# Kernel optimization log

Measured on AMD Instinct MI355X. Metric: run time of the kernel, lower is better.

The kernel has to match this reference:

```python
import jax, jax.numpy as jnp
import numpy as np

K = 32            # spatial kernel: neighbors per anchor
STRIDE = 4        # spatial_stride -> S = N // 4 anchors
TK_HALF = 1       # temporal_kernel_size=3 -> window offsets -1,0,+1


def setup_inputs() -> dict:
    key = jax.random.key(0)
    k1, k2, k3 = jax.random.split(key, 3)
    points = jax.random.normal(k1, (2, 4, 8192, 6), dtype=jnp.float32)
    # conv_d: Conv2d(4 -> 64, 1x1, bias=False) as a dense matrix [out,in]
    Wd = jax.random.normal(k2, (64, 4), dtype=jnp.float32) * 0.1
    # mlp: Conv2d(64 -> 128, 1x1, bias=False)
    Wm = jax.random.normal(k3, (128, 64), dtype=jnp.float32) * 0.1
    return {"points": points, "Wd": Wd, "Wm": Wm}


def _fps(xyz, npoint):
    """Farthest point sampling on a single frame. xyz: [N,3] -> idx [npoint] int32.
    Deterministic start at index 0."""
    d0 = jnp.sum((xyz - xyz[0]) ** 2, axis=-1)  # [N]

    def body(dists, _):
        nxt = jnp.argmax(dists)
        d = jnp.sum((xyz - xyz[nxt]) ** 2, axis=-1)
        return jnp.minimum(dists, d), nxt.astype(jnp.int32)

    _, idxs = jax.lax.scan(body, d0, None, length=npoint - 1)
    return jnp.concatenate([jnp.zeros((1,), jnp.int32), idxs])


def _knn_idx(neighbor_xyz, anchor_xyz, k):
    """Adaptive ball query realized as k-nearest-neighbors.
    neighbor_xyz: [B,N,3], anchor_xyz: [B,S,3] -> idx [B,S,k]."""
    d2 = jnp.sum((anchor_xyz[:, :, None, :] - neighbor_xyz[:, None, :, :]) ** 2, axis=-1)  # [B,S,N]
    _, idx = jax.lax.top_k(-d2, k)
    return idx


def _group(pts, idx):
    """pts: [B,N,C], idx: [B,S,K] -> [B,S,K,C] gather per batch."""
    return jax.vmap(lambda p, i: p[i])(pts, idx)


def reference(points, Wd, Wm):
    xyzs = points[..., :3]                       # [B,L,N,3] (rgb unused when in_planes==0)
    B, L, N, _ = xyzs.shape
    S = N // STRIDE
    # replicate temporal padding [1,1]
    pad = jnp.concatenate([xyzs[:, :1], xyzs, xyzs[:, -1:]], axis=1)  # [B,L+2,N,3]

    new_xyzs, new_feats = [], []
    for t in range(TK_HALF, L + 2 - TK_HALF):    # anchor frames in padded indexing
        frame = pad[:, t]                        # [B,N,3]
        aidx = jax.vmap(lambda x: _fps(x, S))(frame)       # [B,S]
        anchor = _group(frame, aidx[:, :, None])[:, :, 0]  # [B,S,3]

        fsum = jnp.zeros((B, S, Wm.shape[0]), dtype=points.dtype)
        for di in range(-TK_HALF, TK_HALF + 1):
            nb = pad[:, t + di]                              # [B,N,3]
            idx = _knn_idx(nb, anchor, K)                    # [B,S,K]
            grouped = _group(nb, idx)                        # [B,S,K,3]
            disp = grouped - anchor[:, :, None, :]           # xyz displacement
            tdisp = jnp.full((B, S, K, 1), float(di), dtype=points.dtype)
            d4 = jnp.concatenate([disp, tdisp], axis=-1)     # [B,S,K,4]
            h = jax.nn.relu(jnp.einsum('bskc,oc->bsko', d4, Wd))   # conv_d + ReLU
            h = jax.nn.relu(jnp.einsum('bsko,po->bskp', h, Wm))    # mlp + ReLU
            fsum = fsum + jnp.max(h, axis=2)                 # spatial max-pool, temporal sum
        new_xyzs.append(anchor)
        new_feats.append(fsum)

    new_xyzs = jnp.stack(new_xyzs, axis=1)                   # [B,T,S,3]
    new_feats = jnp.stack(new_feats, axis=1).transpose(0, 1, 3, 2)  # [B,T,C,S]
    return new_xyzs, new_feats
```

## Files before the change

### kernel.cpp

```cpp
#include <hip/hip_runtime.h>
#include <stdint.h>

#define NPTS 8192
#define NS   2048
#define KNNK 32

typedef unsigned long long u64;
typedef float f32x2 __attribute__((ext_vector_type(2)));

__device__ __forceinline__ float wave_max_f32_dpp(float x) {
    int t;
    t = __builtin_amdgcn_update_dpp(0, __float_as_int(x), 0xB1, 0xF, 0xF, false);
    x = fmaxf(x, __int_as_float(t));
    t = __builtin_amdgcn_update_dpp(0, __float_as_int(x), 0x4E, 0xF, 0xF, false);
    x = fmaxf(x, __int_as_float(t));
    t = __builtin_amdgcn_update_dpp(0, __float_as_int(x), 0x141, 0xF, 0xF, false);
    x = fmaxf(x, __int_as_float(t));
    t = __builtin_amdgcn_update_dpp(0, __float_as_int(x), 0x140, 0xF, 0xF, false);
    x = fmaxf(x, __int_as_float(t));
    t = __builtin_amdgcn_update_dpp(0, __float_as_int(x), 0x142, 0xF, 0xF, false);
    x = fmaxf(x, __int_as_float(t));
    t = __builtin_amdgcn_update_dpp(0, __float_as_int(x), 0x143, 0xF, 0xF, false);
    x = fmaxf(x, __int_as_float(t));
    return x;
}

__device__ __forceinline__ int wave_min_i32_dpp(int x) {
    const int INF = 0x7FFFFFFF;
    int t;
    t = __builtin_amdgcn_update_dpp(INF, x, 0xB1, 0xF, 0xF, false);
    x = t < x ? t : x;
    t = __builtin_amdgcn_update_dpp(INF, x, 0x4E, 0xF, 0xF, false);
    x = t < x ? t : x;
    t = __builtin_amdgcn_update_dpp(INF, x, 0x141, 0xF, 0xF, false);
    x = t < x ? t : x;
    t = __builtin_amdgcn_update_dpp(INF, x, 0x140, 0xF, 0xF, false);
    x = t < x ? t : x;
    t = __builtin_amdgcn_update_dpp(INF, x, 0x142, 0xF, 0xF, false);
    x = t < x ? t : x;
    t = __builtin_amdgcn_update_dpp(INF, x, 0x143, 0xF, 0xF, false);
    x = t < x ? t : x;
    return x;
}

__global__ __launch_bounds__(512)
void fps_kernel(const float* __restrict__ pts,
                float* __restrict__ out_xyz)
{
#pragma clang fp contract(off)
    const int bt  = blockIdx.x;
    const int tid = threadIdx.x;
    const float* frame = pts + (size_t)bt * NPTS * 6;

    __shared__ float4 p4[NPTS];
    __shared__ u64 ring[3];

    f32x2 x2[8], y2[8], z2[8], dd2[8];
#pragma unroll
    for (int j = 0; j < 16; ++j) {
        int n = j * 512 + tid;
        float x = frame[n*6+0], y = frame[n*6+1], z = frame[n*6+2];
        x2[j >> 1][j & 1] = x;
        y2[j >> 1][j & 1] = y;
        z2[j >> 1][j & 1] = z;
        dd2[j >> 1][j & 1] = 3.4028234663852886e38f;
        p4[n] = make_float4(x, y, z, 0.0f);
    }
    if (tid < 3) ring[tid] = 0;
    if (tid == 0) {
        float* ow = out_xyz + (size_t)bt * NS * 3;
        ow[0] = x2[0][0]; ow[1] = y2[0][0]; ow[2] = z2[0][0];
    }
    __syncthreads();
    float sx = p4[0].x, sy = p4[0].y, sz = p4[0].z;

    int r = 1;
    for (int i = 1; i < NS; ++i) {
        f32x2 sxv = {sx, sx}, syv = {sy, sy}, szv = {sz, sz};
        f32x2 m2 = {0.0f, 0.0f};
#pragma unroll
        for (int q = 0; q < 8; ++q) {
            f32x2 dx = x2[q] - sxv;
            f32x2 dy = y2[q] - syv;
            f32x2 dz = z2[q] - szv;
            f32x2 dd = (dx*dx + dy*dy) + dz*dz;
            f32x2 nd;
            nd[0] = fminf(dd2[q][0], dd[0]);
            nd[1] = fminf(dd2[q][1], dd[1]);
            dd2[q] = nd;
            m2[0] = fmaxf(m2[0], nd[0]);
            m2[1] = fmaxf(m2[1], nd[1]);
        }
        float mloc = fmaxf(m2[0], m2[1]);
        int bestn = 0;
#pragma unroll
        for (int j = 15; j >= 0; --j)
            bestn = (dd2[j >> 1][j & 1] == mloc) ? (j * 512 + tid) : bestn;
        float wM = wave_max_f32_dpp(mloc);
        float M = __int_as_float(__builtin_amdgcn_readlane(__float_as_int(wM), 63));
        int cand = (mloc == M) ? bestn : 0x7FFFFFFF;
        int wI = wave_min_i32_dpp(cand);
        int idxm = __builtin_amdgcn_readlane(wI, 63);
        if ((tid & 63) == 0) {
            u64 key = ((u64)__float_as_uint(M) << 32) | (unsigned)(8191 - idxm);
            atomicMax(&ring[r], key);
        }
        int rn = r + 1; if (rn == 3) rn = 0;
        if (tid == 0) ring[rn] = 0;
        __syncthreads();
        u64 k = ring[r];
        int idx = 8191 - (int)(k & 0xFFFFFFFFu);
        float4 c = p4[idx];
        sx = c.x; sy = c.y; sz = c.z;
        if (tid == 0) {
            float* ow = out_xyz + ((size_t)bt * NS + i) * 3;
            ow[0] = sx; ow[1] = sy; ow[2] = sz;
        }
        r = rn;
    }
}

__device__ __forceinline__ void knn_compact(u64* st, int lane, int& cnt, u64& rk)
{
    for (int e = 0; e < 32; ++e)
        if (e >= cnt) st[(e + 32) * 64 + lane] = ~0ull;
    for (int k = 2; k <= 32; k <<= 1)
        for (int j = k >> 1; j > 0; j >>= 1)
            for (int i = 0; i < 32; ++i) {
                int l = i ^ j;
                if (l > i) {
                    u64 a = st[(i + 32) * 64 + lane];
                    u64 b = st[(l + 32) * 64 + lane];
                    bool asc = ((i & k) == 0);
                    if ((a > b) == asc) {
                        st[(i + 32) * 64 + lane] = b;
                        st[(l + 32) * 64 + lane] = a;
                    }
                }
            }
    for (int i = 0; i < 32; ++i) {
        u64 a = st[i * 64 + lane];
        u64 b = st[(63 - i) * 64 + lane];
        if (b < a) st[i * 64 + lane] = b;
    }
    for (int j = 16; j > 0; j >>= 1)
        for (int i = 0; i < 32; ++i) {
            int l = i ^ j;
            if (l > i) {
                u64 a = st[i * 64 + lane];
                u64 b = st[l * 64 + lane];
                if (a > b) {
                    st[i * 64 + lane] = b;
                    st[l * 64 + lane] = a;
                }
            }
        }
    rk = st[31 * 64 + lane];
    cnt = 0;
}

__global__ __launch_bounds__(64)
void knn_kernel(const float* __restrict__ pts,
                const float* __restrict__ anchors,
                unsigned short* __restrict__ knn_out)
{
    const int blk  = blockIdx.x;
    const int bt   = blk / 96;
    const int r    = blk % 96;
    const int di   = r / 32;
    const int sblk = r % 32;
    const int b = bt >> 2, t0 = bt & 3;
    int lnb = t0 + di - 1; lnb = lnb < 0 ? 0 : (lnb > 3 ? 3 : lnb);
    const float* nb = pts + (size_t)(b * 4 + lnb) * NPTS * 6;
    const int lane = threadIdx.x;
    const int s    = sblk * 64 + lane;

    const float* ap = anchors + ((size_t)bt * NS + s) * 3;
    float ax = ap[0], ay = ap[1], az = ap[2];

    __shared__ u64 st[65 * 64];
    __shared__ float4 tile[512];

    for (int e = 0; e < 64; ++e) st[e * 64 + lane] = ~0ull;
    u64 rk = ~0ull;
    int cnt = 0;

    for (int tb = 0; tb < NPTS; tb += 512) {
        __syncthreads();
#pragma unroll
        for (int q = 0; q < 8; ++q) {
            int c = q * 64 + lane;
            int n = tb + c;
            tile[c] = make_float4(nb[n*6+0], nb[n*6+1], nb[n*6+2], 0.0f);
        }
        __syncthreads();
        for (int c0 = 0; c0 < 512; c0 += 8) {
#pragma unroll
            for (int j = 0; j < 8; ++j) {
                float4 qv = tile[c0 + j];
                float dx = __fsub_rn(ax, qv.x);
                float dy = __fsub_rn(ay, qv.y);
                float dz = __fsub_rn(az, qv.z);
                float d2 = __fadd_rn(__fadd_rn(__fmul_rn(dx,dx), __fmul_rn(dy,dy)),
                                     __fmul_rn(dz,dz));
                u64 key = ((u64)__float_as_uint(d2) << 32)
                        | (unsigned)(tb + c0 + j);
                bool p = key < rk;
                int row = p ? (32 + cnt) : 64;
                st[row * 64 + lane] = key;
                cnt += p ? 1 : 0;
            }
            if (__any(cnt >= 24)) knn_compact(st, lane, cnt, rk);
        }
    }
    knn_compact(st, lane, cnt, rk);

    unsigned short* op = knn_out + (((size_t)bt * 3 + di) * NS + s) * KNNK;
#pragma unroll
    for (int e = 0; e < 32; ++e)
        op[e] = (unsigned short)(st[e * 64 + lane] & 0xFFFFull);
}

__global__ __launch_bounds__(256)
void mlp_kernel(const float* __restrict__ pts,
                const float* __restrict__ anchors,
                const unsigned short* __restrict__ knn,
                const float* __restrict__ Wd,
                const float* __restrict__ Wm,
                float* __restrict__ out_feats)
{
    const int blk   = blockIdx.x;
    const int bt    = blk >> 10;
    const int spair = blk & 1023;
    const int b = bt >> 2, t0 = bt & 3;
    const int tid = threadIdx.x;
    const int a   = tid >> 7;
    const int p   = tid & 127;
    const int s   = spair * 2 + a;

    __shared__ float WmT[64 * 128];
    __shared__ float Wds[256];
    __shared__ float h1[2][64][36];
    __shared__ float d4s[2][32][4];

    for (int i = tid; i < 8192; i += 256) {
        int pp = i >> 6, oo = i & 63;
        WmT[oo * 128 + pp] = Wm[i];
    }
    Wds[tid & 255] = Wd[tid & 255];

    float fsum = 0.0f;

    for (int dd = 0; dd < 3; ++dd) {
        __syncthreads();
        if (tid < 64) {
            int sa = tid >> 5, k = tid & 31;
            int ss = spair * 2 + sa;
            int lnb = t0 + dd - 1; lnb = lnb < 0 ? 0 : (lnb > 3 ? 3 : lnb);
            const float* nbf = pts + (size_t)(b*4 + lnb) * NPTS * 6;
            const float* ap = anchors + ((size_t)bt * NS + ss) * 3;
            int idx = knn[(((size_t)bt*3 + dd) * NS + ss) * KNNK + k];
            d4s[sa][k][0] = nbf[idx*6+0] - ap[0];
            d4s[sa][k][1] = nbf[idx*6+1] - ap[1];
            d4s[sa][k][2] = nbf[idx*6+2] - ap[2];
            d4s[sa][k][3] = (float)(dd - 1);
        }
        __syncthreads();
        {
            int k  = tid & 31;
            int oq = (tid >> 5) & 3;
            float4 dv = *(const float4*)&d4s[a][k][0];
#pragma unroll
            for (int ii = 0; ii < 16; ++ii) {
                int o = oq * 16 + ii;
                float4 w = *(const float4*)&Wds[o * 4];
                float h = fmaf(dv.x, w.x, fmaf(dv.y, w.y, fmaf(dv.z, w.z, dv.w * w.w)));
                h1[a][o][k] = fmaxf(h, 0.0f);
            }
        }
        __syncthreads();
        float acc[32];
#pragma unroll
        for (int kk = 0; kk < 32; ++kk) acc[kk] = 0.0f;
        for (int o = 0; o < 64; ++o) {
            float wmv = WmT[o * 128 + p];
            const float4* hp = (const float4*)&h1[a][o][0];
#pragma unroll
            for (int kk = 0; kk < 8; ++kk) {
                float4 hv = hp[kk];
                acc[kk*4+0] = fmaf(wmv, hv.x, acc[kk*4+0]);
                acc[kk*4+1] = fmaf(wmv, hv.y, acc[kk*4+1]);
                acc[kk*4+2] = fmaf(wmv, hv.z, acc[kk*4+2]);
                acc[kk*4+3] = fmaf(wmv, hv.w, acc[kk*4+3]);
            }
        }
        float mx = acc[0];
#pragma unroll
        for (int kk = 1; kk < 32; ++kk) mx = fmaxf(mx, acc[kk]);
        fsum += fmaxf(mx, 0.0f);
    }
    out_feats[((size_t)bt * 128 + p) * NS + s] = fsum;
}

extern "C" void kernel_launch(void* const* d_in, const int* in_sizes, int n_in,
                              void* d_out, int out_size, void* d_ws, size_t ws_size,
                              hipStream_t stream)
{
    const float* pts = (const float*)d_in[0];
    const float* Wd  = (const float*)d_in[1];
    const float* Wm  = (const float*)d_in[2];

    float* out_xyz   = (float*)d_out;
    float* out_feats = out_xyz + 8 * NS * 3;

    unsigned short* knn = (unsigned short*)d_ws;

    fps_kernel<<<8, 512, 0, stream>>>(pts, out_xyz);
    knn_kernel<<<8 * 3 * 32, 64, 0, stream>>>(pts, out_xyz, knn);
    mlp_kernel<<<8 * (NS / 2), 256, 0, stream>>>(pts, out_xyz, knn, Wd, Wm, out_feats);
}
```

Measured before the change: 2.983 ms.

## Replace FPS atomic ring with per-wave key slots and register-tile MLP

In the FPS kernel, each wave now writes its best key into a double-buffered per-wave slot, and every thread reduces the eight slots after the barrier. This replaces the LDS atomicMax on a rotating ring plus its reset, removing atomic latency from the serial per-iteration critical path. The first-index search is rewritten as a bitmask followed by ctz. In the MLP kernel, each thread now computes a 4-output by 8-neighbor register tile instead of one output across all 32 neighbors, which cuts LDS load traffic per FMA. The price is an extra shared-memory partial-max buffer and an additional barrier per temporal step.

```diff
diff --git a/kernel.cpp b/kernel.cpp
--- a/kernel.cpp
+++ b/kernel.cpp
@@ -53,7 +53,7 @@
     const float* frame = pts + (size_t)bt * NPTS * 6;
 
     __shared__ float4 p4[NPTS];
-    __shared__ u64 ring[3];
+    __shared__ u64 wkey[2][8];
 
     f32x2 x2[8], y2[8], z2[8], dd2[8];
 #pragma unroll
@@ -66,7 +66,6 @@
         dd2[j >> 1][j & 1] = 3.4028234663852886e38f;
         p4[n] = make_float4(x, y, z, 0.0f);
     }
-    if (tid < 3) ring[tid] = 0;
     if (tid == 0) {
         float* ow = out_xyz + (size_t)bt * NS * 3;
         ow[0] = x2[0][0]; ow[1] = y2[0][0]; ow[2] = z2[0][0];
@@ -74,7 +73,6 @@
     __syncthreads();
     float sx = p4[0].x, sy = p4[0].y, sz = p4[0].z;
 
-    int r = 1;
     for (int i = 1; i < NS; ++i) {
         f32x2 sxv = {sx, sx}, syv = {sy, sy}, szv = {sz, sz};
         f32x2 m2 = {0.0f, 0.0f};
@@ -92,23 +90,28 @@
             m2[1] = fmaxf(m2[1], nd[1]);
         }
         float mloc = fmaxf(m2[0], m2[1]);
-        int bestn = 0;
-#pragma unroll
-        for (int j = 15; j >= 0; --j)
-            bestn = (dd2[j >> 1][j & 1] == mloc) ? (j * 512 + tid) : bestn;
+        unsigned mask = 0;
+#pragma unroll
+        for (int j = 0; j < 16; ++j)
+            mask |= (dd2[j >> 1][j & 1] == mloc) ? (1u << j) : 0u;
+        int bestn = __builtin_ctz(mask) * 512 + tid;
         float wM = wave_max_f32_dpp(mloc);
         float M = __int_as_float(__builtin_amdgcn_readlane(__float_as_int(wM), 63));
         int cand = (mloc == M) ? bestn : 0x7FFFFFFF;
         int wI = wave_min_i32_dpp(cand);
         int idxm = __builtin_amdgcn_readlane(wI, 63);
-        if ((tid & 63) == 0) {
-            u64 key = ((u64)__float_as_uint(M) << 32) | (unsigned)(8191 - idxm);
-            atomicMax(&ring[r], key);
-        }
-        int rn = r + 1; if (rn == 3) rn = 0;
-        if (tid == 0) ring[rn] = 0;
-        __syncthreads();
-        u64 k = ring[r];
+        if ((tid & 63) == 0)
+            wkey[i & 1][tid >> 6] =
+                ((u64)__float_as_uint(M) << 32) | (unsigned)(8191 - idxm);
+        __syncthreads();
+        const u64* wk = wkey[i & 1];
+        u64 a0 = wk[0] > wk[1] ? wk[0] : wk[1];
+        u64 a1 = wk[2] > wk[3] ? wk[2] : wk[3];
+        u64 a2 = wk[4] > wk[5] ? wk[4] : wk[5];
+        u64 a3 = wk[6] > wk[7] ? wk[6] : wk[7];
+        u64 b0 = a0 > a1 ? a0 : a1;
+        u64 b1 = a2 > a3 ? a2 : a3;
+        u64 k  = b0 > b1 ? b0 : b1;
         int idx = 8191 - (int)(k & 0xFFFFFFFFu);
         float4 c = p4[idx];
         sx = c.x; sy = c.y; sz = c.z;
@@ -116,7 +119,6 @@
             float* ow = out_xyz + ((size_t)bt * NS + i) * 3;
             ow[0] = sx; ow[1] = sy; ow[2] = sz;
         }
-        r = rn;
     }
 }
 
@@ -235,13 +237,18 @@
     const int b = bt >> 2, t0 = bt & 3;
     const int tid = threadIdx.x;
     const int a   = tid >> 7;
-    const int p   = tid & 127;
+    const int r   = tid & 127;
+    const int pt  = r & 31;
+    const int kt  = r >> 5;
+    const int p   = r;
     const int s   = spair * 2 + a;
+    const int p0  = pt * 4, k0 = kt * 8;
 
     __shared__ float WmT[64 * 128];
     __shared__ float Wds[256];
-    __shared__ float h1[2][64][36];
+    __shared__ float h1[2][64][32];
     __shared__ float d4s[2][32][4];
+    __shared__ float pmax[2][4][128];
 
     for (int i = tid; i < 8192; i += 256) {
         int pp = i >> 6, oo = i & 63;
@@ -279,25 +286,41 @@
             }
         }
         __syncthreads();
-        float acc[32];
-#pragma unroll
-        for (int kk = 0; kk < 32; ++kk) acc[kk] = 0.0f;
+        float acc[4][8];
+#pragma unroll
+        for (int i = 0; i < 4; ++i)
+#pragma unroll
+            for (int j = 0; j < 8; ++j) acc[i][j] = 0.0f;
         for (int o = 0; o < 64; ++o) {
-            float wmv = WmT[o * 128 + p];
-            const float4* hp = (const float4*)&h1[a][o][0];
-#pragma unroll
-            for (int kk = 0; kk < 8; ++kk) {
-                float4 hv = hp[kk];
-                acc[kk*4+0] = fmaf(wmv, hv.x, acc[kk*4+0]);
-                acc[kk*4+1] = fmaf(wmv, hv.y, acc[kk*4+1]);
-                acc[kk*4+2] = fmaf(wmv, hv.z, acc[kk*4+2]);
-                acc[kk*4+3] = fmaf(wmv, hv.w, acc[kk*4+3]);
-            }
-        }
-        float mx = acc[0];
-#pragma unroll
-        for (int kk = 1; kk < 32; ++kk) mx = fmaxf(mx, acc[kk]);
-        fsum += fmaxf(mx, 0.0f);
+            float4 wv = *(const float4*)&WmT[o * 128 + p0];
+            float4 h0 = *(const float4*)&h1[a][o][k0];
+            float4 h4 = *(const float4*)&h1[a][o][k0 + 4];
+#pragma unroll
+            for (int i = 0; i < 4; ++i) {
+                float w = (i == 0) ? wv.x : (i == 1) ? wv.y : (i == 2) ? wv.z : wv.w;
+                acc[i][0] = fmaf(w, h0.x, acc[i][0]);
+                acc[i][1] = fmaf(w, h0.y, acc[i][1]);
+                acc[i][2] = fmaf(w, h0.z, acc[i][2]);
+                acc[i][3] = fmaf(w, h0.w, acc[i][3]);
+                acc[i][4] = fmaf(w, h4.x, acc[i][4]);
+                acc[i][5] = fmaf(w, h4.y, acc[i][5]);
+                acc[i][6] = fmaf(w, h4.z, acc[i][6]);
+                acc[i][7] = fmaf(w, h4.w, acc[i][7]);
+            }
+        }
+        float4 pm;
+#pragma unroll
+        for (int i = 0; i < 4; ++i) {
+            float m = acc[i][0];
+#pragma unroll
+            for (int j = 1; j < 8; ++j) m = fmaxf(m, acc[i][j]);
+            ((float*)&pm)[i] = m;
+        }
+        *(float4*)&pmax[a][kt][p0] = pm;
+        __syncthreads();
+        float m = fmaxf(fmaxf(pmax[a][0][p], pmax[a][1][p]),
+                        fmaxf(pmax[a][2][p], pmax[a][3][p]));
+        fsum += fmaxf(m, 0.0f);
     }
     out_feats[((size_t)bt * 128 + p) * NS + s] = fsum;
 }
```

Result: slower. 3.091 ms (+3.6%).
